# Performance work log

Hardware: AMD Instinct MI355X
Metric: run time of the kernel (lower is better)

## Reference

```python
import jax, jax.numpy as jnp
import numpy as np

N_NODES = 200000
N_EDGES = 3200000
N_FEAT = 128
N_GRAPHS = 1000
N_CLASSES = 10
K = 30          # sort-pool k
C_CAT = 97      # 32+32+32+1 concatenated channels


def _glorot(k, shape):
    fan = shape[0] + shape[-1]
    return jax.random.normal(k, shape, jnp.float32) * (2.0 / fan) ** 0.5


def setup_inputs() -> dict:
    key = jax.random.key(0)
    ks = jax.random.split(key, 20)
    x = jax.random.normal(ks[0], (N_NODES, N_FEAT), jnp.float32)
    edge_index = jax.random.randint(ks[1], (2, N_EDGES), 0, N_NODES, jnp.int32)
    batch = jnp.sort(jax.random.randint(ks[2], (N_NODES,), 0, N_GRAPHS, jnp.int32))
    params = dict(
        W1=_glorot(ks[3], (N_FEAT, 32)), b1=jnp.zeros((32,), jnp.float32),
        W2=_glorot(ks[4], (32, 32)),     b2=jnp.zeros((32,), jnp.float32),
        W3=_glorot(ks[5], (32, 32)),     b3=jnp.zeros((32,), jnp.float32),
        W4=_glorot(ks[6], (32, 1)),      b4=jnp.zeros((1,), jnp.float32),
        conv5_w=_glorot(ks[7], (16, 1, 97)),  conv5_b=jnp.zeros((16,), jnp.float32),
        conv6_w=_glorot(ks[8], (32, 16, 5)),  conv6_b=jnp.zeros((32,), jnp.float32),
        fc1_w=_glorot(ks[9], (352, 128)),     fc1_b=jnp.zeros((128,), jnp.float32),
        fc2_w=_glorot(ks[10], (128, N_CLASSES)), fc2_b=jnp.zeros((N_CLASSES,), jnp.float32),
    )
    return dict(x=x, edge_index=edge_index, batch=batch, **params)


def reference(x, edge_index, batch, W1, b1, W2, b2, W3, b3, W4, b4,
              conv5_w, conv5_b, conv6_w, conv6_b, fc1_w, fc1_b, fc2_w, fc2_b):
    N = x.shape[0]
    src, dst = edge_index[0], edge_index[1]
    emask = (src != dst).astype(x.dtype)            # remove_self_loops
    deg = jax.ops.segment_sum(emask, dst, num_segments=N) + 1.0  # +1 for added self-loop
    inv_sqrt = jax.lax.rsqrt(deg)
    coef = emask * inv_sqrt[src] * inv_sqrt[dst]    # D^-1/2 (A) D^-1/2 edge weight
    inv_deg = 1.0 / deg                             # self-loop weight

    def gcn(h, W, b):
        hw = h @ W
        agg = jax.ops.segment_sum(hw[src] * coef[:, None], dst, num_segments=N)
        return agg + hw * inv_deg[:, None] + b

    x1 = jnp.tanh(gcn(x, W1, b1))
    x2 = jnp.tanh(gcn(x1, W2, b2))
    x3 = jnp.tanh(gcn(x2, W3, b3))
    x4 = jnp.tanh(gcn(x3, W4, b4))
    xc = jnp.concatenate([x1, x2, x3, x4], axis=-1)  # [N, 97]

    # SortAggregation(k=30): per-graph descending sort by last channel, top-k, zero pad
    perm = jnp.lexsort((-xc[:, -1], batch))          # batch-major, last channel desc
    xs, bs = xc[perm], batch[perm]
    counts = jax.ops.segment_sum(jnp.ones_like(batch), batch, num_segments=N_GRAPHS)
    starts = jnp.cumsum(counts) - counts
    rank = jnp.arange(N, dtype=jnp.int32) - starts[bs]
    valid = rank < K
    pooled = jnp.zeros((N_GRAPHS, K, C_CAT), xc.dtype).at[
        bs, jnp.where(valid, rank, K - 1)].add(jnp.where(valid[:, None], xs, 0.0))

    z = pooled.reshape(N_GRAPHS, 1, K * C_CAT)       # [G, 1, 2910]
    dn = ('NCH', 'OIH', 'NCH')
    z = jax.lax.conv_general_dilated(z, conv5_w, (97,), 'VALID', dimension_numbers=dn)
    z = jax.nn.relu(z + conv5_b[None, :, None])      # [G, 16, 30]
    z = jax.lax.reduce_window(z, -jnp.inf, jax.lax.max, (1, 1, 2), (1, 1, 2), 'VALID')
    z = jax.lax.conv_general_dilated(z, conv6_w, (1,), 'VALID', dimension_numbers=dn)
    z = jax.nn.relu(z + conv6_b[None, :, None])      # [G, 32, 11]
    z = z.reshape(N_GRAPHS, -1)                      # [G, 352]
    h = jax.nn.relu(z @ fc1_w + fc1_b)               # dropout is identity in eval
    return jax.nn.log_softmax(h @ fc2_w + fc2_b, axis=-1)
```

## Files before the change

kernel.cpp:

```cpp
#include <hip/hip_runtime.h>
#include <math.h>

#define NN 200000
#define NE 3200000
#define NF 128
#define NG 1000
#define KSEL 30
#define CCAT 97
#define NPAD 200704
#define SCAN_BLKS 196

#define BWID 512
#define NB 391
#define BCAP 10240
#define P1_CHUNK 8192
#define P1_BLKS 391

__global__ void k_p1_partition(const int* __restrict__ ei, int* __restrict__ bcursor,
                               int* __restrict__ ebuf) {
    __shared__ int lhist[NB];
    __shared__ int lbase[NB];
    int tid = threadIdx.x;
    int base = blockIdx.x * P1_CHUNK;
    for (int b = tid; b < NB; b += 256) lhist[b] = 0;
    __syncthreads();
    for (int it = 0; it < P1_CHUNK / 256; it++) {
        int e = base + it * 256 + tid;
        if (e < NE) {
            int s = ei[e], d = ei[NE + e];
            if (s != d) atomicAdd(&lhist[d >> 9], 1);
        }
    }
    __syncthreads();
    for (int b = tid; b < NB; b += 256) {
        int cnt = lhist[b];
        lbase[b] = cnt ? atomicAdd(&bcursor[b], cnt) : 0;
        lhist[b] = 0;
    }
    __syncthreads();
    for (int it = 0; it < P1_CHUNK / 256; it++) {
        int e = base + it * 256 + tid;
        if (e < NE) {
            int s = ei[e], d = ei[NE + e];
            if (s != d) {
                int b = d >> 9;
                int r = atomicAdd(&lhist[b], 1);
                int pos = lbase[b] + r;
                if (pos >= BCAP) pos = BCAP - 1;
                ebuf[b * BCAP + pos] = s | ((d & 511) << 18);
            }
        }
    }
}

__global__ void k_p2_count(const int* __restrict__ bcursor, const int* __restrict__ ebuf,
                           int* __restrict__ rowcnt, float* __restrict__ inv_sqrt) {
    __shared__ int lcnt[BWID];
    int b = blockIdx.x;
    int tid = threadIdx.x;
    for (int i = tid; i < BWID; i += 256) lcnt[i] = 0;
    __syncthreads();
    int size = bcursor[b];
    if (size > BCAP) size = BCAP;
    const int* eb = ebuf + b * BCAP;
    for (int k = tid; k < size; k += 256) atomicAdd(&lcnt[eb[k] >> 18], 1);
    __syncthreads();
    int node0 = b * BWID;
    for (int i = tid; i < BWID; i += 256) {
        int node = node0 + i;
        if (node < NN) {
            int c = lcnt[i];
            rowcnt[node] = c;
            inv_sqrt[node] = rsqrtf((float)(c + 1));
        }
    }
}

__global__ void k_scanA(const int* __restrict__ in, int* __restrict__ out,
                        int* __restrict__ bsums) {
    __shared__ int s[1024];
    int tid = threadIdx.x;
    int gid = blockIdx.x * 1024 + tid;
    int v = in[gid];
    s[tid] = v;
    __syncthreads();
    for (int off = 1; off < 1024; off <<= 1) {
        int a = (tid >= off) ? s[tid - off] : 0;
        int cur = s[tid];
        __syncthreads();
        s[tid] = cur + a;
        __syncthreads();
    }
    out[gid] = s[tid] - v;
    if (tid == 1023) bsums[blockIdx.x] = s[tid];
}

__global__ void k_scanB(int* __restrict__ bsums) {
    __shared__ int s[256];
    int tid = threadIdx.x;
    int v = (tid < SCAN_BLKS) ? bsums[tid] : 0;
    s[tid] = v;
    __syncthreads();
    for (int off = 1; off < 256; off <<= 1) {
        int a = (tid >= off) ? s[tid - off] : 0;
        int cur = s[tid];
        __syncthreads();
        s[tid] = cur + a;
        __syncthreads();
    }
    if (tid < SCAN_BLKS) bsums[tid] = s[tid] - v;
}

__global__ void k_scanC(int* __restrict__ out, const int* __restrict__ bsums) {
    int gid = blockIdx.x * 1024 + threadIdx.x;
    out[gid] += bsums[blockIdx.x];
}

__global__ void k_p3_scatter(const int* __restrict__ bcursor, const int* __restrict__ ebuf,
                             const int* __restrict__ rowstart, int* __restrict__ esrc) {
    __shared__ int lcur[BWID];
    int b = blockIdx.x;
    int tid = threadIdx.x;
    int node0 = b * BWID;
    for (int i = tid; i < BWID; i += 256) lcur[i] = rowstart[node0 + i];
    __syncthreads();
    int size = bcursor[b];
    if (size > BCAP) size = BCAP;
    const int* eb = ebuf + b * BCAP;
    for (int k = tid; k < size; k += 256) {
        int v = eb[k];
        int local = v >> 18;
        int pos = atomicAdd(&lcur[local], 1);
        esrc[pos] = v & 0x3FFFF;
    }
}

template <int K>
__global__ void k_mm(const float* __restrict__ X, const float* __restrict__ W,
                     const float* __restrict__ inv_sqrt, float* __restrict__ Y) {
    __shared__ float4 sW[K * 8];
    int tid = threadIdx.x;
    for (int i = tid; i < K * 8; i += 256) sW[i] = ((const float4*)W)[i];
    __syncthreads();
    int row = blockIdx.x * 256 + tid;
    if (row >= NN) return;
    float s = inv_sqrt[row];
    const float4* xp = (const float4*)(X + (size_t)row * K);
    float4 acc[8];
#pragma unroll
    for (int q = 0; q < 8; q++) acc[q] = make_float4(0.f, 0.f, 0.f, 0.f);
#pragma unroll 2
    for (int k4 = 0; k4 < K / 4; k4++) {
        float4 xv = xp[k4];
        const float4* wk = &sW[k4 * 32];
#pragma unroll
        for (int kk = 0; kk < 4; kk++) {
            float xs = (kk == 0) ? xv.x : (kk == 1) ? xv.y : (kk == 2) ? xv.z : xv.w;
#pragma unroll
            for (int q = 0; q < 8; q++) {
                float4 w = wk[kk * 8 + q];
                acc[q].x = fmaf(xs, w.x, acc[q].x);
                acc[q].y = fmaf(xs, w.y, acc[q].y);
                acc[q].z = fmaf(xs, w.z, acc[q].z);
                acc[q].w = fmaf(xs, w.w, acc[q].w);
            }
        }
    }
    float4* yp = (float4*)(Y + (size_t)row * 32);
#pragma unroll
    for (int q = 0; q < 8; q++) {
        float4 v = acc[q];
        v.x *= s; v.y *= s; v.z *= s; v.w *= s;
        yp[q] = v;
    }
}

__global__ void k_aggr(const int* __restrict__ rowstart, const int* __restrict__ esrc,
                       const float* __restrict__ hws, const float* __restrict__ inv_sqrt,
                       const float* __restrict__ b, float* __restrict__ xout) {
    int t = blockIdx.x * 256 + threadIdx.x;
    int n = t >> 5, c = t & 31;
    if (n >= NN) return;
    int e0 = rowstart[n], e1 = rowstart[n + 1];
    float a[8];
    a[0] = hws[(size_t)n * 32 + c];
#pragma unroll
    for (int k = 1; k < 8; k++) a[k] = 0.0f;
    for (int e = e0; e < e1; e += 8) {
        int ss[8];
#pragma unroll
        for (int k = 0; k < 8; k++) ss[k] = esrc[(e + k < e1) ? e + k : e];
        float vv[8];
#pragma unroll
        for (int k = 0; k < 8; k++) vv[k] = hws[(size_t)ss[k] * 32 + c];
        a[0] += vv[0];
#pragma unroll
        for (int k = 1; k < 8; k++) a[k] += (e + k < e1) ? vv[k] : 0.0f;
    }
    float acc = ((a[0] + a[1]) + (a[2] + a[3])) + ((a[4] + a[5]) + (a[6] + a[7]));
    xout[t] = tanhf(fmaf(acc, inv_sqrt[n], b[c]));
}

__global__ void k_mm4(const float* __restrict__ x3, const float* __restrict__ W4,
                      const float* __restrict__ inv_sqrt, float* __restrict__ hws4) {
    int n = blockIdx.x * 256 + threadIdx.x;
    if (n >= NN) return;
    const float4* xr = (const float4*)(x3 + (size_t)n * 32);
    float acc = 0.0f;
#pragma unroll
    for (int q = 0; q < 8; q++) {
        float4 v = xr[q];
        acc = fmaf(v.x, W4[q * 4 + 0], acc);
        acc = fmaf(v.y, W4[q * 4 + 1], acc);
        acc = fmaf(v.z, W4[q * 4 + 2], acc);
        acc = fmaf(v.w, W4[q * 4 + 3], acc);
    }
    hws4[n] = acc * inv_sqrt[n];
}

__global__ void k_aggr1(const int* __restrict__ rowstart, const int* __restrict__ esrc,
                        const float* __restrict__ hws4, const float* __restrict__ inv_sqrt,
                        const float* __restrict__ b4, float* __restrict__ x4) {
    int n = blockIdx.x * 256 + threadIdx.x;
    if (n >= NN) return;
    int e0 = rowstart[n], e1 = rowstart[n + 1];
    float a[8];
    a[0] = hws4[n];
#pragma unroll
    for (int k = 1; k < 8; k++) a[k] = 0.0f;
    for (int e = e0; e < e1; e += 8) {
        int ss[8];
#pragma unroll
        for (int k = 0; k < 8; k++) ss[k] = esrc[(e + k < e1) ? e + k : e];
        float vv[8];
#pragma unroll
        for (int k = 0; k < 8; k++) vv[k] = hws4[ss[k]];
        a[0] += vv[0];
#pragma unroll
        for (int k = 1; k < 8; k++) a[k] += (e + k < e1) ? vv[k] : 0.0f;
    }
    float acc = ((a[0] + a[1]) + (a[2] + a[3])) + ((a[4] + a[5]) + (a[6] + a[7]));
    x4[n] = tanhf(fmaf(acc, inv_sqrt[n], b4[0]));
}

__global__ void k_gbounds(const int* __restrict__ batch, int* __restrict__ starts) {
    int n = blockIdx.x * 256 + threadIdx.x;
    if (n >= NN) return;
    int bn = batch[n];
    int bp = (n == 0) ? -1 : batch[n - 1];
    for (int g = bp + 1; g <= bn; g++) starts[g] = n;
    if (n == NN - 1)
        for (int g = bn + 1; g <= NG; g++) starts[g] = NN;
}

__global__ void k_sortpool(const int* __restrict__ starts,
                           const float* __restrict__ x1, const float* __restrict__ x2,
                           const float* __restrict__ x3, const float* __restrict__ x4,
                           float* __restrict__ pooled) {
    __shared__ float keys[1024];
    __shared__ int sel[KSEL];
    int g = blockIdx.x;
    int tid = threadIdx.x;
    int start = starts[g];
    int cnt = starts[g + 1] - start;
    if (cnt > 1024) cnt = 1024;
    for (int i = tid; i < cnt; i += 256) keys[i] = x4[start + i];
    __syncthreads();
    for (int i = tid; i < cnt; i += 256) {
        float ki = keys[i];
        int rank = 0;
        for (int j = 0; j < cnt; j++) {
            float kj = keys[j];
            rank += (kj > ki) || (kj == ki && j < i);
        }
        if (rank < KSEL) sel[rank] = start + i;
    }
    __syncthreads();
    int selcnt = cnt < KSEL ? cnt : KSEL;
    for (int t = tid; t < KSEL * CCAT; t += 256) {
        int r = t / CCAT, ch = t - r * CCAT;
        float v = 0.0f;
        if (r < selcnt) {
            int node = sel[r];
            if (ch < 32)      v = x1[(size_t)node * 32 + ch];
            else if (ch < 64) v = x2[(size_t)node * 32 + ch - 32];
            else if (ch < 96) v = x3[(size_t)node * 32 + ch - 64];
            else              v = x4[node];
        }
        pooled[g * (KSEL * CCAT) + t] = v;
    }
}

__global__ void k_head(const float* __restrict__ pooled,
                       const float* __restrict__ w5, const float* __restrict__ b5,
                       const float* __restrict__ w6, const float* __restrict__ b6,
                       const float* __restrict__ fw1, const float* __restrict__ fb1,
                       const float* __restrict__ fw2, const float* __restrict__ fb2,
                       float* __restrict__ out) {
    __shared__ float sP[KSEL * CCAT];
    __shared__ float s5[16 * 30];
    __shared__ float smp[16 * 15];
    __shared__ float sz[352];
    __shared__ float sh[128];
    __shared__ float sl[10];
    int g = blockIdx.x;
    int tid = threadIdx.x;
    for (int i = tid; i < KSEL * CCAT; i += 256) sP[i] = pooled[g * (KSEL * CCAT) + i];
    __syncthreads();
    for (int t = tid; t < 16 * 30; t += 256) {
        int c = t / 30, j = t - c * 30;
        float acc = b5[c];
        for (int i = 0; i < CCAT; i++) acc = fmaf(sP[j * CCAT + i], w5[c * CCAT + i], acc);
        s5[c * 30 + j] = fmaxf(acc, 0.0f);
    }
    __syncthreads();
    for (int t = tid; t < 16 * 15; t += 256) {
        int c = t / 15, j = t - c * 15;
        smp[t] = fmaxf(s5[c * 30 + 2 * j], s5[c * 30 + 2 * j + 1]);
    }
    __syncthreads();
    for (int t = tid; t < 32 * 11; t += 256) {
        int c = t / 11, j = t - c * 11;
        float acc = b6[c];
        for (int ci = 0; ci < 16; ci++) {
#pragma unroll
            for (int k = 0; k < 5; k++)
                acc = fmaf(smp[ci * 15 + j + k], w6[(c * 16 + ci) * 5 + k], acc);
        }
        sz[t] = fmaxf(acc, 0.0f);
    }
    __syncthreads();
    if (tid < 128) {
        float acc = fb1[tid];
        for (int i = 0; i < 352; i++) acc = fmaf(sz[i], fw1[i * 128 + tid], acc);
        sh[tid] = fmaxf(acc, 0.0f);
    }
    __syncthreads();
    if (tid < 10) {
        float acc = fb2[tid];
        for (int i = 0; i < 128; i++) acc = fmaf(sh[i], fw2[i * 10 + tid], acc);
        sl[tid] = acc;
    }
    __syncthreads();
    if (tid < 10) {
        float m = -1e30f;
        for (int i = 0; i < 10; i++) m = fmaxf(m, sl[i]);
        float ssum = 0.0f;
        for (int i = 0; i < 10; i++) ssum += expf(sl[i] - m);
        out[g * 10 + tid] = sl[tid] - m - logf(ssum);
    }
}

extern "C" void kernel_launch(void* const* d_in, const int* in_sizes, int n_in,
                              void* d_out, int out_size, void* d_ws, size_t ws_size,
                              hipStream_t stream) {
    const float* x   = (const float*)d_in[0];
    const int*   ei  = (const int*)d_in[1];
    const int*   bat = (const int*)d_in[2];
    const float* W1  = (const float*)d_in[3];
    const float* b1  = (const float*)d_in[4];
    const float* W2  = (const float*)d_in[5];
    const float* b2  = (const float*)d_in[6];
    const float* W3  = (const float*)d_in[7];
    const float* b3  = (const float*)d_in[8];
    const float* W4  = (const float*)d_in[9];
    const float* b4  = (const float*)d_in[10];
    const float* w5  = (const float*)d_in[11];
    const float* b5  = (const float*)d_in[12];
    const float* w6  = (const float*)d_in[13];
    const float* b6  = (const float*)d_in[14];
    const float* fw1 = (const float*)d_in[15];
    const float* fb1 = (const float*)d_in[16];
    const float* fw2 = (const float*)d_in[17];
    const float* fb2 = (const float*)d_in[18];
    float* out = (float*)d_out;

    float* ws = (float*)d_ws;
    float* inv_sqrt = ws;
    float* hws      = inv_sqrt + NN;
    float* x1       = hws + (size_t)NN * 32;
    float* x2       = x1 + (size_t)NN * 32;
    float* x3       = x2 + (size_t)NN * 32;
    float* x4       = x3 + (size_t)NN * 32;
    float* pooled   = x4 + NN;
    int* rowcnt     = (int*)(pooled + NG * KSEL * CCAT);
    int* rowstart   = rowcnt + NPAD;
    int* esrc       = rowstart + NPAD;
    int* bcursor    = esrc + NE;
    int* bsums      = bcursor + 512;
    int* gstarts    = bsums + 256;
    int* ebuf       = (int*)x3;

    const int TB = 256;
    int gN  = (NN + TB - 1) / TB;
    int gNC = (NN * 32 + TB - 1) / TB;

    hipMemsetAsync(bcursor, 0, 512 * sizeof(int), stream);
    hipMemsetAsync(rowcnt, 0, NPAD * sizeof(int), stream);
    k_p1_partition<<<P1_BLKS, TB, 0, stream>>>(ei, bcursor, ebuf);
    k_p2_count<<<NB, TB, 0, stream>>>(bcursor, ebuf, rowcnt, inv_sqrt);
    k_scanA<<<SCAN_BLKS, 1024, 0, stream>>>(rowcnt, rowstart, bsums);
    k_scanB<<<1, 256, 0, stream>>>(bsums);
    k_scanC<<<SCAN_BLKS, 1024, 0, stream>>>(rowstart, bsums);
    k_p3_scatter<<<NB, TB, 0, stream>>>(bcursor, ebuf, rowstart, esrc);

    k_gbounds<<<gN, TB, 0, stream>>>(bat, gstarts);

    k_mm<128><<<gN, TB, 0, stream>>>(x, W1, inv_sqrt, hws);
    k_aggr<<<gNC, TB, 0, stream>>>(rowstart, esrc, hws, inv_sqrt, b1, x1);
    k_mm<32><<<gN, TB, 0, stream>>>(x1, W2, inv_sqrt, hws);
    k_aggr<<<gNC, TB, 0, stream>>>(rowstart, esrc, hws, inv_sqrt, b2, x2);
    k_mm<32><<<gN, TB, 0, stream>>>(x2, W3, inv_sqrt, hws);
    k_aggr<<<gNC, TB, 0, stream>>>(rowstart, esrc, hws, inv_sqrt, b3, x3);
    k_mm4<<<gN, TB, 0, stream>>>(x3, W4, inv_sqrt, hws);
    k_aggr1<<<gN, TB, 0, stream>>>(rowstart, esrc, hws, inv_sqrt, b4, x4);

    k_sortpool<<<NG, TB, 0, stream>>>(gstarts, x1, x2, x3, x4, pooled);
    k_head<<<NG, TB, 0, stream>>>(pooled, w5, b5, w6, b6, fw1, fb1, fw2, fb2, out);
}
```

Baseline: 614.8 us.

## Retile dense GCN matmul so 8 threads share rows, each computing four output columns

The node-feature matmul kernel changes from one thread per row computing all 32 outputs to groups of 8 threads, each computing a 4-column slice for 4 rows. Each block now covers 128 rows, and the launch grid is adjusted to match. The aim is to cut per-thread register pressure and raise occupancy (launch bounds set for 6 blocks), while keeping every X element reused across 4 outputs per thread. In exchange, each X row is now loaded by 8 threads, relying on cache or broadcast, and the X reads become strided across lanes, which may hurt coalescing.

```diff
diff --git a/kernel.cpp b/kernel.cpp
--- a/kernel.cpp
+++ b/kernel.cpp
@@ -136,43 +136,62 @@
 }
 
 template <int K>
-__global__ void k_mm(const float* __restrict__ X, const float* __restrict__ W,
-                     const float* __restrict__ inv_sqrt, float* __restrict__ Y) {
+__global__ void __launch_bounds__(256, 6) k_mm(const float* __restrict__ X,
+                                               const float* __restrict__ W,
+                                               const float* __restrict__ inv_sqrt,
+                                               float* __restrict__ Y) {
     __shared__ float4 sW[K * 8];
     int tid = threadIdx.x;
     for (int i = tid; i < K * 8; i += 256) sW[i] = ((const float4*)W)[i];
     __syncthreads();
-    int row = blockIdx.x * 256 + tid;
-    if (row >= NN) return;
-    float s = inv_sqrt[row];
-    const float4* xp = (const float4*)(X + (size_t)row * K);
-    float4 acc[8];
-#pragma unroll
-    for (int q = 0; q < 8; q++) acc[q] = make_float4(0.f, 0.f, 0.f, 0.f);
+    int g = tid >> 3;
+    int q = tid & 7;
+    int r0 = blockIdx.x * 128 + g * 4;
+    if (r0 >= NN) return;
+    const float4* __restrict__ xp0 = (const float4*)(X + (size_t)(r0 + 0) * K);
+    const float4* __restrict__ xp1 = (const float4*)(X + (size_t)(r0 + 1) * K);
+    const float4* __restrict__ xp2 = (const float4*)(X + (size_t)(r0 + 2) * K);
+    const float4* __restrict__ xp3 = (const float4*)(X + (size_t)(r0 + 3) * K);
+    float4 a0 = make_float4(0.f, 0.f, 0.f, 0.f);
+    float4 a1 = make_float4(0.f, 0.f, 0.f, 0.f);
+    float4 a2 = make_float4(0.f, 0.f, 0.f, 0.f);
+    float4 a3 = make_float4(0.f, 0.f, 0.f, 0.f);
 #pragma unroll 2
     for (int k4 = 0; k4 < K / 4; k4++) {
-        float4 xv = xp[k4];
-        const float4* wk = &sW[k4 * 32];
+        float4 x0 = xp0[k4];
+        float4 x1 = xp1[k4];
+        float4 x2 = xp2[k4];
+        float4 x3 = xp3[k4];
+        const float4* wk = &sW[k4 * 32 + q];
 #pragma unroll
         for (int kk = 0; kk < 4; kk++) {
-            float xs = (kk == 0) ? xv.x : (kk == 1) ? xv.y : (kk == 2) ? xv.z : xv.w;
-#pragma unroll
-            for (int q = 0; q < 8; q++) {
-                float4 w = wk[kk * 8 + q];
-                acc[q].x = fmaf(xs, w.x, acc[q].x);
-                acc[q].y = fmaf(xs, w.y, acc[q].y);
-                acc[q].z = fmaf(xs, w.z, acc[q].z);
-                acc[q].w = fmaf(xs, w.w, acc[q].w);
-            }
-        }
-    }
-    float4* yp = (float4*)(Y + (size_t)row * 32);
-#pragma unroll
-    for (int q = 0; q < 8; q++) {
-        float4 v = acc[q];
-        v.x *= s; v.y *= s; v.z *= s; v.w *= s;
-        yp[q] = v;
-    }
+            float4 w = wk[kk * 8];
+            float s0 = (kk == 0) ? x0.x : (kk == 1) ? x0.y : (kk == 2) ? x0.z : x0.w;
+            float s1 = (kk == 0) ? x1.x : (kk == 1) ? x1.y : (kk == 2) ? x1.z : x1.w;
+            float s2 = (kk == 0) ? x2.x : (kk == 1) ? x2.y : (kk == 2) ? x2.z : x2.w;
+            float s3 = (kk == 0) ? x3.x : (kk == 1) ? x3.y : (kk == 2) ? x3.z : x3.w;
+            a0.x = fmaf(s0, w.x, a0.x); a0.y = fmaf(s0, w.y, a0.y);
+            a0.z = fmaf(s0, w.z, a0.z); a0.w = fmaf(s0, w.w, a0.w);
+            a1.x = fmaf(s1, w.x, a1.x); a1.y = fmaf(s1, w.y, a1.y);
+            a1.z = fmaf(s1, w.z, a1.z); a1.w = fmaf(s1, w.w, a1.w);
+            a2.x = fmaf(s2, w.x, a2.x); a2.y = fmaf(s2, w.y, a2.y);
+            a2.z = fmaf(s2, w.z, a2.z); a2.w = fmaf(s2, w.w, a2.w);
+            a3.x = fmaf(s3, w.x, a3.x); a3.y = fmaf(s3, w.y, a3.y);
+            a3.z = fmaf(s3, w.z, a3.z); a3.w = fmaf(s3, w.w, a3.w);
+        }
+    }
+    float s0 = inv_sqrt[r0 + 0];
+    float s1 = inv_sqrt[r0 + 1];
+    float s2 = inv_sqrt[r0 + 2];
+    float s3 = inv_sqrt[r0 + 3];
+    a0.x *= s0; a0.y *= s0; a0.z *= s0; a0.w *= s0;
+    a1.x *= s1; a1.y *= s1; a1.z *= s1; a1.w *= s1;
+    a2.x *= s2; a2.y *= s2; a2.z *= s2; a2.w *= s2;
+    a3.x *= s3; a3.y *= s3; a3.z *= s3; a3.w *= s3;
+    ((float4*)(Y + (size_t)(r0 + 0) * 32))[q] = a0;
+    ((float4*)(Y + (size_t)(r0 + 1) * 32))[q] = a1;
+    ((float4*)(Y + (size_t)(r0 + 2) * 32))[q] = a2;
+    ((float4*)(Y + (size_t)(r0 + 3) * 32))[q] = a3;
 }
 
 __global__ void k_aggr(const int* __restrict__ rowstart, const int* __restrict__ esrc,
@@ -394,6 +413,7 @@
     const int TB = 256;
     int gN  = (NN + TB - 1) / TB;
     int gNC = (NN * 32 + TB - 1) / TB;
+    int gMM = (NN + 127) / 128;
 
     hipMemsetAsync(bcursor, 0, 512 * sizeof(int), stream);
     hipMemsetAsync(rowcnt, 0, NPAD * sizeof(int), stream);
@@ -406,11 +426,11 @@
 
     k_gbounds<<<gN, TB, 0, stream>>>(bat, gstarts);
 
-    k_mm<128><<<gN, TB, 0, stream>>>(x, W1, inv_sqrt, hws);
+    k_mm<128><<<gMM, TB, 0, stream>>>(x, W1, inv_sqrt, hws);
     k_aggr<<<gNC, TB, 0, stream>>>(rowstart, esrc, hws, inv_sqrt, b1, x1);
-    k_mm<32><<<gN, TB, 0, stream>>>(x1, W2, inv_sqrt, hws);
+    k_mm<32><<<gMM, TB, 0, stream>>>(x1, W2, inv_sqrt, hws);
     k_aggr<<<gNC, TB, 0, stream>>>(rowstart, esrc, hws, inv_sqrt, b2, x2);
-    k_mm<32><<<gN, TB, 0, stream>>>(x2, W3, inv_sqrt, hws);
+    k_mm<32><<<gMM, TB, 0, stream>>>(x2, W3, inv_sqrt, hws);
     k_aggr<<<gNC, TB, 0, stream>>>(rowstart, esrc, hws, inv_sqrt, b3, x3);
     k_mm4<<<gN, TB, 0, stream>>>(x3, W4, inv_sqrt, hws);
     k_aggr1<<<gN, TB, 0, stream>>>(rowstart, esrc, hws, inv_sqrt, b4, x4);
```

Measured after the change: 597.1 us. 1.03x faster.
